# Kernel tuning notes

Measured on AMD Instinct MI355X. Metric: run time of the kernel, lower is better.

Reference implementation:

```python
import jax, jax.numpy as jnp
import numpy as np

HIDDEN = 4096
NUM_HEADS = 32
NUM_KV_HEADS = 8
HEAD_DIM = 128
EPS = 1e-6
ROPE_THETA = 1000000.0
B, S = 4, 1024


def setup_inputs() -> dict:
    key = jax.random.key(0)
    ks = jax.random.split(key, 8)
    sd = 1.0 / np.sqrt(HIDDEN)
    return {
        "hidden_states": jax.random.normal(ks[0], (B, S, HIDDEN), jnp.float32),
        "positions": jnp.broadcast_to(jnp.arange(S, dtype=jnp.int32), (B, S)),
        "wq": jax.random.normal(ks[1], (HIDDEN, NUM_HEADS * HEAD_DIM), jnp.float32) * sd,
        "wk": jax.random.normal(ks[2], (HIDDEN, NUM_KV_HEADS * HEAD_DIM), jnp.float32) * sd,
        "wv": jax.random.normal(ks[3], (HIDDEN, NUM_KV_HEADS * HEAD_DIM), jnp.float32) * sd,
        "wo": jax.random.normal(ks[4], (NUM_HEADS * HEAD_DIM, HIDDEN), jnp.float32) * sd,
        "q_norm_scale": jnp.ones((HEAD_DIM,), jnp.float32),
        "k_norm_scale": jnp.ones((HEAD_DIM,), jnp.float32),
    }


def _rms_norm(x, scale):
    # per-head RMSNorm over last dim (head_dim)
    var = jnp.mean(jnp.square(x), axis=-1, keepdims=True)
    return x * jax.lax.rsqrt(var + EPS) * scale


def _rope_non_neox(x, positions):
    # x: [B, S, H, D]; non-neox (interleaved) RoPE over full head_dim
    inv_freq = 1.0 / (ROPE_THETA ** (jnp.arange(0, HEAD_DIM, 2, dtype=jnp.float32) / HEAD_DIM))
    freqs = positions.astype(jnp.float32)[..., None] * inv_freq  # [B, S, D/2]
    cos = jnp.cos(freqs)[:, :, None, :]  # [B, S, 1, D/2]
    sin = jnp.sin(freqs)[:, :, None, :]
    x1 = x[..., 0::2]
    x2 = x[..., 1::2]
    o1 = x1 * cos - x2 * sin
    o2 = x2 * cos + x1 * sin
    return jnp.stack([o1, o2], axis=-1).reshape(x.shape)


def reference(hidden_states, positions, wq, wk, wv, wo, q_norm_scale, k_norm_scale):
    b, s, _ = hidden_states.shape
    q = (hidden_states @ wq).reshape(b, s, NUM_HEADS, HEAD_DIM)
    k = (hidden_states @ wk).reshape(b, s, NUM_KV_HEADS, HEAD_DIM)
    v = (hidden_states @ wv).reshape(b, s, NUM_KV_HEADS, HEAD_DIM)

    q = _rms_norm(q, q_norm_scale)
    k = _rms_norm(k, k_norm_scale)

    q = _rope_non_neox(q, positions)
    k = _rope_non_neox(k, positions)

    # GQA: expand kv heads to match q heads
    group = NUM_HEADS // NUM_KV_HEADS
    k = jnp.repeat(k, group, axis=2)  # [B, S, NH, D]
    v = jnp.repeat(v, group, axis=2)

    scale = HEAD_DIM ** -0.5
    scores = jnp.einsum("bqhd,bkhd->bhqk", q, k) * scale  # [B, NH, S, S]
    causal = jnp.tril(jnp.ones((s, s), dtype=bool))
    scores = jnp.where(causal, scores, jnp.finfo(scores.dtype).min)
    probs = jax.nn.softmax(scores, axis=-1)
    attn = jnp.einsum("bhqk,bkhd->bqhd", probs, v).reshape(b, s, NUM_HEADS * HEAD_DIM)
    return attn @ wo
```

## Files before the change

kernel.cpp:

```cpp
#include <hip/hip_runtime.h>
#include <hip/hip_bf16.h>
#include <cstdint>

#define HIDDEN 4096
#define NQ 32
#define NKV 8
#define HD 128
#define BB 4
#define SS 1024
#define NTOK (BB*SS)
#define NQKV 6144

typedef __bf16 bf16x8 __attribute__((ext_vector_type(8)));
typedef float f32x4 __attribute__((ext_vector_type(4)));
typedef unsigned short u16;
typedef unsigned int u32;

__device__ __forceinline__ void gload_lds16(const void* g, void* l) {
  __builtin_amdgcn_global_load_lds((const __attribute__((address_space(1))) u32*)g,
                                   (__attribute__((address_space(3))) u32*)l, 16, 0, 0);
}

__device__ __forceinline__ u16 f2bf(float f) {
  u32 x = __float_as_uint(f);
  u32 r = x + 0x7fffu + ((x >> 16) & 1u);
  return (u16)(r >> 16);
}
__device__ __forceinline__ float bf2f(u16 x) {
  u32 v = ((u32)x) << 16;
  return __uint_as_float(v);
}

__global__ void cast_f32_bf16_k(const float4* __restrict__ in, ushort4* __restrict__ out, int n4)
{
  for (int i = blockIdx.x*blockDim.x + threadIdx.x; i < n4; i += gridDim.x*blockDim.x) {
    float4 v = in[i];
    ushort4 o;
    o.x = f2bf(v.x); o.y = f2bf(v.y); o.z = f2bf(v.z); o.w = f2bf(v.w);
    out[i] = o;
  }
}

__global__ __launch_bounds__(256) void transpose_cast(const float* __restrict__ in,
                                                      u16* __restrict__ out, int K, int N)
{
  __shared__ float tile[32][33];
  int n0 = blockIdx.x*32, k0 = blockIdx.y*32;
  int tx = threadIdx.x & 31, ty = threadIdx.x >> 5;
  #pragma unroll
  for (int i=0;i<4;i++) {
    int k = ty + i*8;
    tile[k][tx] = in[(size_t)(k0+k)*N + n0 + tx];
  }
  __syncthreads();
  #pragma unroll
  for (int i=0;i<4;i++) {
    int n = ty + i*8;
    out[(size_t)(n0+n)*K + k0 + tx] = f2bf(tile[tx][n]);
  }
}

__global__ void rope_tab_k(const int* __restrict__ pos, float2* __restrict__ tab)
{
  int i = blockIdx.x*256 + threadIdx.x;
  if (i >= NTOK*64) return;
  int t = i >> 6, j = i & 63;
  float p = (float)pos[t];
  const float l2t = 19.931568569324174f;
  float inv = exp2f(-(float)j * (l2t/64.0f));
  float f = p * inv;
  tab[i] = make_float2(cosf(f), sinf(f));
}

template<int BF16_OUT>
__global__ __launch_bounds__(256, 2) void gemm_bt(const u16* __restrict__ A,
                                                  const u16* __restrict__ Bt,
                                                  void* __restrict__ Cv,
                                                  int M, int N, int K)
{
  __shared__ u16 lA[128*64];
  __shared__ u16 lB[128*64];
  const int m0 = blockIdx.y*128, n0 = blockIdx.x*128;
  const int tid = threadIdx.x;
  const int w = tid >> 6, l = tid & 63;
  const int wr = w >> 1, wc = w & 1;
  const int cl = l & 15, g4 = l >> 4;
  const int lr = l >> 3, gd = l & 7;
  f32x4 acc[4][4] = {};

  for (int k0 = 0; k0 < K; k0 += 64) {
    #pragma unroll
    for (int c2 = 0; c2 < 4; ++c2) {
      int r = w*32 + c2*8 + lr;
      int gs = gd ^ (r & 7);
      gload_lds16(A  + (size_t)(m0+r)*K + k0 + gs*8, &lA[(w*32 + c2*8)*64]);
      gload_lds16(Bt + (size_t)(n0+r)*K + k0 + gs*8, &lB[(w*32 + c2*8)*64]);
    }
    __syncthreads();
    #pragma unroll
    for (int kk = 0; kk < 2; ++kk) {
      bf16x8 af[4], bfr[4];
      #pragma unroll
      for (int i=0;i<4;i++) {
        int ra = wr*64 + i*16 + cl;
        af[i]  = *(const bf16x8*)&lA[ra*64 + ((kk*4+g4) ^ (ra&7))*8];
        int rb = wc*64 + i*16 + cl;
        bfr[i] = *(const bf16x8*)&lB[rb*64 + ((kk*4+g4) ^ (rb&7))*8];
      }
      #pragma unroll
      for (int i=0;i<4;i++)
        #pragma unroll
        for (int j=0;j<4;j++)
          acc[i][j] = __builtin_amdgcn_mfma_f32_16x16x32_bf16(af[i], bfr[j], acc[i][j], 0,0,0);
    }
    __syncthreads();
  }

  #pragma unroll
  for (int i=0;i<4;i++)
    #pragma unroll
    for (int rg=0;rg<4;rg++) {
      size_t row = m0 + wr*64 + i*16 + g4*4 + rg;
      #pragma unroll
      for (int j=0;j<4;j++) {
        size_t col = n0 + wc*64 + j*16 + cl;
        if (BF16_OUT) ((u16*)Cv)[row*N + col] = f2bf(acc[i][j][rg]);
        else          ((float*)Cv)[row*N + col] = acc[i][j][rg];
      }
    }
}

__global__ __launch_bounds__(256) void norm_rope(u16* __restrict__ qkv,
                                                 const float* __restrict__ qsc,
                                                 const float* __restrict__ ksc,
                                                 const float2* __restrict__ tab)
{
  const int t = blockIdx.x;
  const int w = threadIdx.x >> 6, l = threadIdx.x & 63;
  const float2 cs = tab[t*64 + l];
  for (int slot = w; slot < 40; slot += 4) {
    const float* sc = (slot < 32) ? qsc : ksc;
    int col = (slot < 32) ? slot*HD : 4096 + (slot-32)*HD;
    u32* p = (u32*)(qkv + (size_t)t*NQKV + col) + l;
    u32 v = *p;
    float x0 = bf2f((u16)(v & 0xffff)), x1 = bf2f((u16)(v >> 16));
    float ss = x0*x0 + x1*x1;
    ss += __shfl_xor(ss, 1);  ss += __shfl_xor(ss, 2);  ss += __shfl_xor(ss, 4);
    ss += __shfl_xor(ss, 8);  ss += __shfl_xor(ss, 16); ss += __shfl_xor(ss, 32);
    float r = rsqrtf(ss * (1.0f/128.0f) + 1e-6f);
    float y0 = x0 * r * sc[2*l], y1 = x1 * r * sc[2*l+1];
    float o0 = y0*cs.x - y1*cs.y;
    float o1 = y1*cs.x + y0*cs.y;
    *p = (u32)f2bf(o0) | ((u32)f2bf(o1) << 16);
  }
}

__global__ __launch_bounds__(256) void v_transpose(const u16* __restrict__ qkv,
                                                   u16* __restrict__ vt)
{
  __shared__ u16 tile[32][136];
  const int s0 = blockIdx.x*32;
  const int z  = blockIdx.y;
  const int b = z >> 3, kvh = z & 7;
  const int tid = threadIdx.x;
  const int tr = tid >> 4, ln = tid & 15;
  const size_t base = ((size_t)b*SS)*NQKV + 5120 + (size_t)kvh*HD;
  #pragma unroll
  for (int i=0;i<2;i++) {
    int srow = tr + i*16;
    *(bf16x8*)&tile[srow][ln*8] =
        *(const bf16x8*)&qkv[base + (size_t)(s0+srow)*NQKV + ln*8];
  }
  __syncthreads();
  const int dr = tid >> 1, sh = (tid & 1)*16;
  u16 tmp[16];
  #pragma unroll
  for (int j=0;j<16;j++) tmp[j] = tile[sh+j][dr];
  u16* o = vt + ((size_t)z*HD + dr)*SS + s0 + sh;
  *(bf16x8*)o       = *(const bf16x8*)&tmp[0];
  *(bf16x8*)(o + 8) = *(const bf16x8*)&tmp[8];
}

__global__ __launch_bounds__(256, 2) void attn_fwd(const u16* __restrict__ qkv,
                                                   const u16* __restrict__ vt,
                                                   u16* __restrict__ out)
{
  __shared__ u16 Kb[2][64*128];
  __shared__ u16 Vb[2][128*64];
  __shared__ u16 Pl[4][16*64];
  const int qp = blockIdx.x, h = blockIdx.y, b = blockIdx.z;
  const int kvh = h >> 2;
  const int tid = threadIdx.x, w = tid >> 6, l = tid & 63;
  const int cl = l & 15, g4 = l >> 4;
  const float csc = 1.4426950408889634f * 0.08838834764831845f;
  const size_t kbase = ((size_t)b*SS)*NQKV + 4096 + (size_t)kvh*HD;
  const size_t vbase = ((size_t)b*8 + (size_t)kvh)*HD*SS;
  u16* Pw = &Pl[w][0];

  const int kr_l = l >> 4, kg_l = l & 15;
  const int vr_l = l >> 3, vg_l = l & 7;

  #pragma unroll
  for (int t = 0; t < 2; ++t) {
    const int qt = t ? (15 - qp) : qp;
    const int q0 = qt*64;

    bf16x8 qf[4];
    const size_t qrow = ((size_t)b*SS + q0 + w*16 + cl)*NQKV + h*HD;
    #pragma unroll
    for (int kk=0;kk<4;kk++) qf[kk] = *(const bf16x8*)&qkv[qrow + kk*32 + g4*8];

    f32x4 O[8] = {};
    float mrow[4] = {-INFINITY,-INFINITY,-INFINITY,-INFINITY};
    float srow[4] = {0.f,0.f,0.f,0.f};

    const int nch = qt + 1;

    #pragma unroll
    for (int i=0;i<4;i++) {
      int inst = w*4 + i;
      int r = inst*4 + kr_l;
      int g = kg_l ^ (r & 15);
      gload_lds16(qkv + kbase + (size_t)r*NQKV + g*8, &Kb[0][inst*512]);
      int d = inst*8 + vr_l;
      int gv = vg_l ^ (d & 7);
      gload_lds16(vt + vbase + (size_t)d*SS + gv*8, &Vb[0][inst*512]);
    }
    __syncthreads();
    int cur = 0;

    for (int ch = 0; ch < nch; ++ch) {
      const int kv0 = ch*64;
      if (ch + 1 < nch) {
        const size_t knext = kbase + (size_t)(kv0+64)*NQKV;
        const size_t vnext = vbase + (size_t)(kv0+64);
        u16* Kn = &Kb[cur^1][0];
        u16* Vn = &Vb[cur^1][0];
        #pragma unroll
        for (int i=0;i<4;i++) {
          int inst = w*4 + i;
          int r = inst*4 + kr_l;
          int g = kg_l ^ (r & 15);
          gload_lds16(qkv + knext + (size_t)r*NQKV + g*8, Kn + inst*512);
          int d = inst*8 + vr_l;
          int gv = vg_l ^ (d & 7);
          gload_lds16(vt + vnext + (size_t)d*SS + gv*8, Vn + inst*512);
        }
      }
      const u16* Kt  = &Kb[cur][0];
      const u16* Vtl = &Vb[cur][0];
      f32x4 s[4] = {};
      #pragma unroll
      for (int cc=0;cc<4;cc++) {
        const int kro = (cc*16+cl)*128;
        #pragma unroll
        for (int kk=0;kk<4;kk++) {
          bf16x8 kf = *(const bf16x8*)&Kt[kro + (((kk*4+g4) ^ cl))*8];
          s[cc] = __builtin_amdgcn_mfma_f32_16x16x32_bf16(qf[kk], kf, s[cc], 0,0,0);
        }
      }
      float alpha[4];
      #pragma unroll
      for (int rg=0; rg<4; ++rg) {
        const int qr = q0 + w*16 + g4*4 + rg;
        float sv[4];
        #pragma unroll
        for (int cc=0;cc<4;cc++) {
          sv[cc] = s[cc][rg]*csc;
          if (kv0 + cc*16 + cl > qr) sv[cc] = -INFINITY;
        }
        float mx = fmaxf(fmaxf(sv[0],sv[1]), fmaxf(sv[2],sv[3]));
        mx = fmaxf(mx, __shfl_xor(mx,1));
        mx = fmaxf(mx, __shfl_xor(mx,2));
        mx = fmaxf(mx, __shfl_xor(mx,4));
        mx = fmaxf(mx, __shfl_xor(mx,8));
        float mn = fmaxf(mrow[rg], mx);
        float al = exp2f(mrow[rg] - mn);
        mrow[rg] = mn;
        float p0 = exp2f(sv[0]-mn), p1 = exp2f(sv[1]-mn);
        float p2 = exp2f(sv[2]-mn), p3 = exp2f(sv[3]-mn);
        float ps = (p0+p1)+(p2+p3);
        ps += __shfl_xor(ps,1); ps += __shfl_xor(ps,2);
        ps += __shfl_xor(ps,4); ps += __shfl_xor(ps,8);
        srow[rg] = srow[rg]*al + ps;
        alpha[rg] = al;
        const int r = g4*4+rg;
        const int rs = r*64, rx = r&7;
        float pv[4] = {p0,p1,p2,p3};
        #pragma unroll
        for (int cc=0;cc<4;cc++) {
          int c = cc*16+cl;
          Pw[rs + (((c>>3) ^ rx))*8 + (c&7)] = f2bf(pv[cc]);
        }
      }
      #pragma unroll
      for (int dc=0;dc<8;dc++)
        #pragma unroll
        for (int rg=0;rg<4;rg++) O[dc][rg] *= alpha[rg];
      #pragma unroll
      for (int cc2=0;cc2<2;cc2++) {
        bf16x8 pf = *(const bf16x8*)&Pw[cl*64 + (((cc2*4+g4) ^ (cl&7)))*8];
        #pragma unroll
        for (int dc=0;dc<8;dc++) {
          bf16x8 vf = *(const bf16x8*)&Vtl[(dc*16+cl)*64 + (((cc2*4+g4) ^ (cl&7)))*8];
          O[dc] = __builtin_amdgcn_mfma_f32_16x16x32_bf16(pf, vf, O[dc], 0,0,0);
        }
      }
      __syncthreads();
      cur ^= 1;
    }
    #pragma unroll
    for (int rg=0;rg<4;rg++) {
      float inv = 1.0f / srow[rg];
      size_t ob = ((size_t)b*SS + q0 + w*16 + g4*4 + rg)*4096 + (size_t)h*HD;
      #pragma unroll
      for (int dc=0;dc<8;dc++)
        out[ob + dc*16 + cl] = f2bf(O[dc][rg]*inv);
    }
  }
}

extern "C" void kernel_launch(void* const* d_in, const int* in_sizes, int n_in,
                              void* d_out, int out_size, void* d_ws, size_t ws_size,
                              hipStream_t stream)
{
  const float* hid = (const float*)d_in[0];
  const int*   pos = (const int*)d_in[1];
  const float* wq  = (const float*)d_in[2];
  const float* wk  = (const float*)d_in[3];
  const float* wv  = (const float*)d_in[4];
  const float* wo  = (const float*)d_in[5];
  const float* qsc = (const float*)d_in[6];
  const float* ksc = (const float*)d_in[7];

  char* ws = (char*)d_ws;
  size_t off = 0;
  auto alloc = [&](size_t b) -> char* {
    char* p = ws + off;
    off = (off + b + 255) & ~(size_t)255;
    return p;
  };
  u16*    h_bf   = (u16*)   alloc((size_t)NTOK*HIDDEN*2);
  u16*    wqkv_t = (u16*)   alloc((size_t)NQKV*HIDDEN*2);
  u16*    wo_t   = (u16*)   alloc((size_t)HIDDEN*HIDDEN*2);
  u16*    qkv    = (u16*)   alloc((size_t)NTOK*NQKV*2);
  u16*    attn_o = (u16*)   alloc((size_t)NTOK*HIDDEN*2);
  u16*    vtb    = (u16*)   alloc((size_t)BB*NKV*HD*SS*2);
  float2* tab    = (float2*)alloc((size_t)NTOK*64*sizeof(float2));

  cast_f32_bf16_k<<<2048, 256, 0, stream>>>((const float4*)hid, (ushort4*)h_bf, NTOK*HIDDEN/4);
  transpose_cast<<<dim3(HIDDEN/32, HIDDEN/32), 256, 0, stream>>>(wq, wqkv_t, HIDDEN, HIDDEN);
  transpose_cast<<<dim3(1024/32,  HIDDEN/32), 256, 0, stream>>>(wk, wqkv_t + (size_t)4096*HIDDEN, HIDDEN, 1024);
  transpose_cast<<<dim3(1024/32,  HIDDEN/32), 256, 0, stream>>>(wv, wqkv_t + (size_t)5120*HIDDEN, HIDDEN, 1024);
  transpose_cast<<<dim3(HIDDEN/32, HIDDEN/32), 256, 0, stream>>>(wo, wo_t, HIDDEN, HIDDEN);
  rope_tab_k<<<NTOK*64/256, 256, 0, stream>>>(pos, tab);

  gemm_bt<1><<<dim3(NQKV/128, NTOK/128), 256, 0, stream>>>(h_bf, wqkv_t, qkv, NTOK, NQKV, HIDDEN);
  norm_rope<<<NTOK, 256, 0, stream>>>(qkv, qsc, ksc, tab);
  v_transpose<<<dim3(SS/32, BB*NKV), 256, 0, stream>>>(qkv, vtb);
  attn_fwd<<<dim3(8, NQ, BB), 256, 0, stream>>>(qkv, vtb, attn_o);
  gemm_bt<0><<<dim3(HIDDEN/128, NTOK/128), 256, 0, stream>>>(attn_o, wo_t, d_out, NTOK, HIDDEN, HIDDEN);
}
```

Measured before the change: 515.3 us.

## Replace GEMM with 256x256 tile, 8-wave, double-buffered LDS pipeline

Swaps the 128x128 single-buffered GEMM for a 256x256-tile kernel with 512 threads (8 waves, each owning a 128x64 output region). LDS is double-buffered and the next K-tile's global-to-LDS loads are issued between MFMA phases, with s_setprio raising wave priority around the MFMA bursts. The aim is more data reuse per tile and to hide global-load latency behind matrix math. In exchange it uses 128 KB of LDS per block, which limits occupancy, and the grids shrink (384 and 256 blocks), which may leave some CUs idle.

```diff
diff --git a/kernel.cpp b/kernel.cpp
--- a/kernel.cpp
+++ b/kernel.cpp
@@ -73,59 +73,129 @@
 }
 
 template<int BF16_OUT>
-__global__ __launch_bounds__(256, 2) void gemm_bt(const u16* __restrict__ A,
-                                                  const u16* __restrict__ Bt,
-                                                  void* __restrict__ Cv,
-                                                  int M, int N, int K)
-{
-  __shared__ u16 lA[128*64];
-  __shared__ u16 lB[128*64];
-  const int m0 = blockIdx.y*128, n0 = blockIdx.x*128;
+__global__ __launch_bounds__(512, 2) void gemm_bt8(const u16* __restrict__ A,
+                                                   const u16* __restrict__ Bt,
+                                                   void* __restrict__ Cv,
+                                                   int M, int N, int K)
+{
+  __shared__ u16 lA[2][256*64];
+  __shared__ u16 lB[2][256*64];
+  const int m0 = blockIdx.y*256, n0 = blockIdx.x*256;
   const int tid = threadIdx.x;
-  const int w = tid >> 6, l = tid & 63;
-  const int wr = w >> 1, wc = w & 1;
+  const int w = tid >> 6;
+  const int wm = w >> 2, wn = w & 3;
+  const int l = tid & 63;
   const int cl = l & 15, g4 = l >> 4;
-  const int lr = l >> 3, gd = l & 7;
-  f32x4 acc[4][4] = {};
-
-  for (int k0 = 0; k0 < K; k0 += 64) {
-    #pragma unroll
-    for (int c2 = 0; c2 < 4; ++c2) {
-      int r = w*32 + c2*8 + lr;
-      int gs = gd ^ (r & 7);
-      gload_lds16(A  + (size_t)(m0+r)*K + k0 + gs*8, &lA[(w*32 + c2*8)*64]);
-      gload_lds16(Bt + (size_t)(n0+r)*K + k0 + gs*8, &lB[(w*32 + c2*8)*64]);
-    }
+  const int rr = tid >> 3;
+  const int sx = (tid & 7) ^ (rr & 7);
+
+  f32x4 acc[8][4] = {};
+  const int nt = K >> 6;
+
+#define STAGE_A(buf, i, k0v) \
+  gload_lds16(A  + (size_t)(m0 + (i)*64 + rr)*K + (k0v) + sx*8, &lA[buf][((i)*64 + w*8)*64])
+#define STAGE_B(buf, i, k0v) \
+  gload_lds16(Bt + (size_t)(n0 + (i)*64 + rr)*K + (k0v) + sx*8, &lB[buf][((i)*64 + w*8)*64])
+
+  #pragma unroll
+  for (int i=0;i<4;i++) { STAGE_A(0,i,0); STAGE_B(0,i,0); }
+  __syncthreads();
+
+  #pragma unroll 2
+  for (int t = 0; t < nt; ++t) {
+    const int cur = t & 1;
+    const int kn = (t+1) << 6;
+    const u16* At = &lA[cur][0];
+    const u16* Bl = &lB[cur][0];
+    bf16x8 a[4][2], b0[2][2], b1[2][2];
+
+    #pragma unroll
+    for (int fi=0;fi<4;fi++) {
+      const int ra = (wm*128 + fi*16 + cl)*64;
+      #pragma unroll
+      for (int kk=0;kk<2;kk++)
+        a[fi][kk] = *(const bf16x8*)&At[ra + (((kk*4+g4) ^ (cl&7)))*8];
+    }
+    #pragma unroll
+    for (int fj=0;fj<2;fj++) {
+      const int rb = (wn*64 + fj*16 + cl)*64;
+      #pragma unroll
+      for (int kk=0;kk<2;kk++)
+        b0[fj][kk] = *(const bf16x8*)&Bl[rb + (((kk*4+g4) ^ (cl&7)))*8];
+    }
+    if (t+1 < nt) { STAGE_A(cur^1,0,kn); STAGE_A(cur^1,1,kn); STAGE_B(cur^1,0,kn); STAGE_B(cur^1,1,kn); }
     __syncthreads();
-    #pragma unroll
-    for (int kk = 0; kk < 2; ++kk) {
-      bf16x8 af[4], bfr[4];
-      #pragma unroll
-      for (int i=0;i<4;i++) {
-        int ra = wr*64 + i*16 + cl;
-        af[i]  = *(const bf16x8*)&lA[ra*64 + ((kk*4+g4) ^ (ra&7))*8];
-        int rb = wc*64 + i*16 + cl;
-        bfr[i] = *(const bf16x8*)&lB[rb*64 + ((kk*4+g4) ^ (rb&7))*8];
-      }
-      #pragma unroll
-      for (int i=0;i<4;i++)
-        #pragma unroll
-        for (int j=0;j<4;j++)
-          acc[i][j] = __builtin_amdgcn_mfma_f32_16x16x32_bf16(af[i], bfr[j], acc[i][j], 0,0,0);
-    }
+    __builtin_amdgcn_s_setprio(1);
+    #pragma unroll
+    for (int fi=0;fi<4;fi++)
+      #pragma unroll
+      for (int fj=0;fj<2;fj++)
+        #pragma unroll
+        for (int kk=0;kk<2;kk++)
+          acc[fi][fj] = __builtin_amdgcn_mfma_f32_16x16x32_bf16(a[fi][kk], b0[fj][kk], acc[fi][fj], 0,0,0);
+    __builtin_amdgcn_s_setprio(0);
+
+    #pragma unroll
+    for (int fj=0;fj<2;fj++) {
+      const int rb = (wn*64 + (fj+2)*16 + cl)*64;
+      #pragma unroll
+      for (int kk=0;kk<2;kk++)
+        b1[fj][kk] = *(const bf16x8*)&Bl[rb + (((kk*4+g4) ^ (cl&7)))*8];
+    }
+    if (t+1 < nt) { STAGE_A(cur^1,2,kn); STAGE_A(cur^1,3,kn); STAGE_B(cur^1,2,kn); STAGE_B(cur^1,3,kn); }
     __syncthreads();
-  }
-
-  #pragma unroll
-  for (int i=0;i<4;i++)
+    __builtin_amdgcn_s_setprio(1);
+    #pragma unroll
+    for (int fi=0;fi<4;fi++)
+      #pragma unroll
+      for (int fj=0;fj<2;fj++)
+        #pragma unroll
+        for (int kk=0;kk<2;kk++)
+          acc[fi][fj+2] = __builtin_amdgcn_mfma_f32_16x16x32_bf16(a[fi][kk], b1[fj][kk], acc[fi][fj+2], 0,0,0);
+    __builtin_amdgcn_s_setprio(0);
+
+    #pragma unroll
+    for (int fi=0;fi<4;fi++) {
+      const int ra = (wm*128 + 64 + fi*16 + cl)*64;
+      #pragma unroll
+      for (int kk=0;kk<2;kk++)
+        a[fi][kk] = *(const bf16x8*)&At[ra + (((kk*4+g4) ^ (cl&7)))*8];
+    }
+    __syncthreads();
+    __builtin_amdgcn_s_setprio(1);
+    #pragma unroll
+    for (int fi=0;fi<4;fi++)
+      #pragma unroll
+      for (int fj=0;fj<2;fj++)
+        #pragma unroll
+        for (int kk=0;kk<2;kk++)
+          acc[fi+4][fj+2] = __builtin_amdgcn_mfma_f32_16x16x32_bf16(a[fi][kk], b1[fj][kk], acc[fi+4][fj+2], 0,0,0);
+    __builtin_amdgcn_s_setprio(0);
+
+    __builtin_amdgcn_s_setprio(1);
+    #pragma unroll
+    for (int fi=0;fi<4;fi++)
+      #pragma unroll
+      for (int fj=0;fj<2;fj++)
+        #pragma unroll
+        for (int kk=0;kk<2;kk++)
+          acc[fi+4][fj] = __builtin_amdgcn_mfma_f32_16x16x32_bf16(a[fi][kk], b0[fj][kk], acc[fi+4][fj], 0,0,0);
+    __builtin_amdgcn_s_setprio(0);
+    __syncthreads();
+  }
+#undef STAGE_A
+#undef STAGE_B
+
+  #pragma unroll
+  for (int am=0;am<8;am++)
     #pragma unroll
     for (int rg=0;rg<4;rg++) {
-      size_t row = m0 + wr*64 + i*16 + g4*4 + rg;
-      #pragma unroll
-      for (int j=0;j<4;j++) {
-        size_t col = n0 + wc*64 + j*16 + cl;
-        if (BF16_OUT) ((u16*)Cv)[row*N + col] = f2bf(acc[i][j][rg]);
-        else          ((float*)Cv)[row*N + col] = acc[i][j][rg];
+      const size_t row = m0 + wm*128 + (am>>2)*64 + (am&3)*16 + g4*4 + rg;
+      #pragma unroll
+      for (int an=0;an<4;an++) {
+        const size_t col = n0 + wn*64 + an*16 + cl;
+        if (BF16_OUT) ((u16*)Cv)[row*N + col] = f2bf(acc[am][an][rg]);
+        else          ((float*)Cv)[row*N + col] = acc[am][an][rg];
       }
     }
 }
@@ -355,9 +425,9 @@
   transpose_cast<<<dim3(HIDDEN/32, HIDDEN/32), 256, 0, stream>>>(wo, wo_t, HIDDEN, HIDDEN);
   rope_tab_k<<<NTOK*64/256, 256, 0, stream>>>(pos, tab);
 
-  gemm_bt<1><<<dim3(NQKV/128, NTOK/128), 256, 0, stream>>>(h_bf, wqkv_t, qkv, NTOK, NQKV, HIDDEN);
+  gemm_bt8<1><<<dim3(NQKV/256, NTOK/256), 512, 0, stream>>>(h_bf, wqkv_t, qkv, NTOK, NQKV, HIDDEN);
   norm_rope<<<NTOK, 256, 0, stream>>>(qkv, qsc, ksc, tab);
   v_transpose<<<dim3(SS/32, BB*NKV), 256, 0, stream>>>(qkv, vtb);
   attn_fwd<<<dim3(8, NQ, BB), 256, 0, stream>>>(qkv, vtb, attn_o);
-  gemm_bt<0><<<dim3(HIDDEN/128, NTOK/128), 256, 0, stream>>>(attn_o, wo_t, d_out, NTOK, HIDDEN, HIDDEN);
-}
+  gemm_bt8<0><<<dim3(HIDDEN/256, NTOK/256), 512, 0, stream>>>(attn_o, wo_t, d_out, NTOK, HIDDEN, HIDDEN);
+}
```

After: 696.2 us. +35.1%, slower.

## Replace GEMM with 256x256 8-wave double-buffered ping-pong pipelined kernel

Applied to the files above, without the earlier changes.

Swaps the 128x128 single-buffered 4-wave GEMM for a 256x256 tile kernel with 8 waves and double-buffered LDS. Loads for the next K-tile are issued in quarters between MFMA phases, and s_setprio plus explicit vmcnt waits overlap global-to-LDS traffic with matrix math. The larger tile raises reuse per loaded byte. In exchange LDS use grows to 128KB per block, which caps occupancy, and fewer blocks are launched (384 and 256), which may underfill the CUs.

```diff
diff --git a/kernel.cpp b/kernel.cpp
--- a/kernel.cpp
+++ b/kernel.cpp
@@ -73,59 +73,110 @@
 }
 
 template<int BF16_OUT>
-__global__ __launch_bounds__(256, 2) void gemm_bt(const u16* __restrict__ A,
-                                                  const u16* __restrict__ Bt,
-                                                  void* __restrict__ Cv,
-                                                  int M, int N, int K)
-{
-  __shared__ u16 lA[128*64];
-  __shared__ u16 lB[128*64];
-  const int m0 = blockIdx.y*128, n0 = blockIdx.x*128;
+__global__ __launch_bounds__(512, 2) void gemm8p(const u16* __restrict__ A,
+                                                 const u16* __restrict__ Bt,
+                                                 void* __restrict__ Cv,
+                                                 int M, int N, int K)
+{
+  __shared__ u16 lA[2][2][128*64];
+  __shared__ u16 lB[2][2][128*64];
+  const int m0 = blockIdx.y*256, n0 = blockIdx.x*256;
   const int tid = threadIdx.x;
   const int w = tid >> 6, l = tid & 63;
-  const int wr = w >> 1, wc = w & 1;
+  const int wm = w >> 2, wn = w & 3;
   const int cl = l & 15, g4 = l >> 4;
-  const int lr = l >> 3, gd = l & 7;
-  f32x4 acc[4][4] = {};
-
-  for (int k0 = 0; k0 < K; k0 += 64) {
-    #pragma unroll
-    for (int c2 = 0; c2 < 4; ++c2) {
-      int r = w*32 + c2*8 + lr;
-      int gs = gd ^ (r & 7);
-      gload_lds16(A  + (size_t)(m0+r)*K + k0 + gs*8, &lA[(w*32 + c2*8)*64]);
-      gload_lds16(Bt + (size_t)(n0+r)*K + k0 + gs*8, &lB[(w*32 + c2*8)*64]);
-    }
-    __syncthreads();
-    #pragma unroll
-    for (int kk = 0; kk < 2; ++kk) {
-      bf16x8 af[4], bfr[4];
-      #pragma unroll
-      for (int i=0;i<4;i++) {
-        int ra = wr*64 + i*16 + cl;
-        af[i]  = *(const bf16x8*)&lA[ra*64 + ((kk*4+g4) ^ (ra&7))*8];
-        int rb = wc*64 + i*16 + cl;
-        bfr[i] = *(const bf16x8*)&lB[rb*64 + ((kk*4+g4) ^ (rb&7))*8];
-      }
-      #pragma unroll
-      for (int i=0;i<4;i++)
-        #pragma unroll
-        for (int j=0;j<4;j++)
-          acc[i][j] = __builtin_amdgcn_mfma_f32_16x16x32_bf16(af[i], bfr[j], acc[i][j], 0,0,0);
-    }
-    __syncthreads();
-  }
-
-  #pragma unroll
-  for (int i=0;i<4;i++)
+  const int sr = l >> 3;
+  const int sg = (l & 7) ^ sr;
+  const u16* Ab = A  + (size_t)m0*K;
+  const u16* Bb = Bt + (size_t)n0*K;
+
+  f32x4 acc[8][4] = {};
+  const int nt = K >> 6;
+
+#define STG_A(buf, half, kt) do { \
+    gload_lds16(Ab + (size_t)((half)*128 +      w*8 + sr)*K + (kt)*64 + sg*8, &lA[buf][half][(     w*8)*64]); \
+    gload_lds16(Ab + (size_t)((half)*128 + 64 + w*8 + sr)*K + (kt)*64 + sg*8, &lA[buf][half][(64 + w*8)*64]); \
+  } while(0)
+#define STG_B(buf, half, kt) do { \
+    gload_lds16(Bb + (size_t)((half)*128 +      w*8 + sr)*K + (kt)*64 + sg*8, &lB[buf][half][(     w*8)*64]); \
+    gload_lds16(Bb + (size_t)((half)*128 + 64 + w*8 + sr)*K + (kt)*64 + sg*8, &lB[buf][half][(64 + w*8)*64]); \
+  } while(0)
+
+#define RD_A(dst, buf, half) \
+    _Pragma("unroll") for (int fi=0;fi<4;fi++) { \
+      const int ra = (wm*64 + fi*16 + cl)*64; \
+      _Pragma("unroll") for (int kk=0;kk<2;kk++) \
+        dst[fi][kk] = *(const bf16x8*)&lA[buf][half][ra + (((kk*4+g4) ^ (cl&7)))*8]; \
+    }
+#define RD_B(dst, buf, half) \
+    _Pragma("unroll") for (int fj=0;fj<2;fj++) { \
+      const int rb = (wn*32 + fj*16 + cl)*64; \
+      _Pragma("unroll") for (int kk=0;kk<2;kk++) \
+        dst[fj][kk] = *(const bf16x8*)&lB[buf][half][rb + (((kk*4+g4) ^ (cl&7)))*8]; \
+    }
+#define MFMA_Q(ai, aj, afrag, bfrag) \
+    __builtin_amdgcn_s_setprio(1); \
+    _Pragma("unroll") for (int fi=0;fi<4;fi++) \
+      _Pragma("unroll") for (int fj=0;fj<2;fj++) \
+        _Pragma("unroll") for (int kk=0;kk<2;kk++) \
+          acc[(ai)+fi][(aj)+fj] = __builtin_amdgcn_mfma_f32_16x16x32_bf16(afrag[fi][kk], bfrag[fj][kk], acc[(ai)+fi][(aj)+fj], 0,0,0); \
+    __builtin_amdgcn_s_setprio(0);
+#define BAR() { __builtin_amdgcn_s_barrier(); __builtin_amdgcn_sched_barrier(0); }
+
+  STG_A(0,0,0); STG_B(0,0,0); STG_A(0,1,0); STG_B(0,1,0);
+  asm volatile("s_waitcnt vmcnt(4)" ::: "memory");
+  BAR();
+
+  for (int t = 0; t < nt; ++t) {
+    const int cur = t & 1, nxt = cur ^ 1;
+    const int kn = t + 1;
+    const bool pf = (kn < nt);
+    bf16x8 aF[4][2], bL[2][2], bH[2][2];
+
+    RD_A(aF, cur, 0);
+    RD_B(bL, cur, 0);
+    if (pf) STG_A(nxt, 0, kn);
+    BAR();
+    MFMA_Q(0, 0, aF, bL);
+    if (pf) { asm volatile("s_waitcnt vmcnt(2)" ::: "memory"); }
+    else    { asm volatile("s_waitcnt vmcnt(0)" ::: "memory"); }
+    BAR();
+
+    RD_B(bH, cur, 1);
+    if (pf) STG_B(nxt, 0, kn);
+    BAR();
+    MFMA_Q(0, 2, aF, bH);
+    BAR();
+
+    RD_A(aF, cur, 1);
+    if (pf) STG_A(nxt, 1, kn);
+    BAR();
+    MFMA_Q(4, 2, aF, bH);
+    BAR();
+
+    if (pf) STG_B(nxt, 1, kn);
+    BAR();
+    MFMA_Q(4, 0, aF, bL);
+    if (pf) { asm volatile("s_waitcnt vmcnt(4)" ::: "memory"); }
+    BAR();
+  }
+#undef STG_A
+#undef STG_B
+#undef RD_A
+#undef RD_B
+#undef MFMA_Q
+#undef BAR
+
+  #pragma unroll
+  for (int am=0;am<8;am++)
     #pragma unroll
     for (int rg=0;rg<4;rg++) {
-      size_t row = m0 + wr*64 + i*16 + g4*4 + rg;
-      #pragma unroll
-      for (int j=0;j<4;j++) {
-        size_t col = n0 + wc*64 + j*16 + cl;
-        if (BF16_OUT) ((u16*)Cv)[row*N + col] = f2bf(acc[i][j][rg]);
-        else          ((float*)Cv)[row*N + col] = acc[i][j][rg];
+      const size_t row = m0 + (am>>2)*128 + wm*64 + (am&3)*16 + g4*4 + rg;
+      #pragma unroll
+      for (int an=0;an<4;an++) {
+        const size_t col = n0 + (an>>1)*128 + wn*32 + (an&1)*16 + cl;
+        if (BF16_OUT) ((u16*)Cv)[row*N + col] = f2bf(acc[am][an][rg]);
+        else          ((float*)Cv)[row*N + col] = acc[am][an][rg];
       }
     }
 }
@@ -355,9 +406,9 @@
   transpose_cast<<<dim3(HIDDEN/32, HIDDEN/32), 256, 0, stream>>>(wo, wo_t, HIDDEN, HIDDEN);
   rope_tab_k<<<NTOK*64/256, 256, 0, stream>>>(pos, tab);
 
-  gemm_bt<1><<<dim3(NQKV/128, NTOK/128), 256, 0, stream>>>(h_bf, wqkv_t, qkv, NTOK, NQKV, HIDDEN);
+  gemm8p<1><<<dim3(NQKV/256, NTOK/256), 512, 0, stream>>>(h_bf, wqkv_t, qkv, NTOK, NQKV, HIDDEN);
   norm_rope<<<NTOK, 256, 0, stream>>>(qkv, qsc, ksc, tab);
   v_transpose<<<dim3(SS/32, BB*NKV), 256, 0, stream>>>(qkv, vtb);
   attn_fwd<<<dim3(8, NQ, BB), 256, 0, stream>>>(qkv, vtb, attn_o);
-  gemm_bt<0><<<dim3(HIDDEN/128, NTOK/128), 256, 0, stream>>>(attn_o, wo_t, d_out, NTOK, HIDDEN, HIDDEN);
-}
+  gemm8p<0><<<dim3(HIDDEN/256, NTOK/256), 512, 0, stream>>>(attn_o, wo_t, d_out, NTOK, HIDDEN, HIDDEN);
+}
```

Result: slower. 543.2 us (+5.4%).

## Replace GEMM with 256x256-tile double-buffered kernel and XCD-aware block swizzle

Applied to the files above, without the earlier changes.

Swaps the 128x128 single-buffered bf16 GEMM for a 256x256-tile kernel with 512 threads. It prefetches K-tiles two steps ahead into double-buffered LDS, using raw s_waitcnt and barriers to overlap loads with MFMA work. Block indices are remapped so consecutive tiles land on the same XCD chiplet, which should improve L2 reuse. The larger tile raises arithmetic intensity, but it uses 128KB of LDS and 128 accumulator registers per thread. That may limit occupancy, and the grids are small (384 and 256 blocks), which risks poor load balance across 256 CUs.

```diff
diff --git a/kernel.cpp b/kernel.cpp
--- a/kernel.cpp
+++ b/kernel.cpp
@@ -73,59 +73,107 @@
 }
 
 template<int BF16_OUT>
-__global__ __launch_bounds__(256, 2) void gemm_bt(const u16* __restrict__ A,
-                                                  const u16* __restrict__ Bt,
-                                                  void* __restrict__ Cv,
-                                                  int M, int N, int K)
-{
-  __shared__ u16 lA[128*64];
-  __shared__ u16 lB[128*64];
-  const int m0 = blockIdx.y*128, n0 = blockIdx.x*128;
+__global__ __launch_bounds__(512, 2) void gemm2b(const u16* __restrict__ A,
+                                                 const u16* __restrict__ Bt,
+                                                 void* __restrict__ Cv,
+                                                 int M, int N, int K, int gx)
+{
+  __shared__ u16 lA[2][256*64];
+  __shared__ u16 lB[2][256*64];
+  const int nwg = gridDim.x;
+  const int cpx = nwg >> 3;
+  const int swz = (blockIdx.x & 7)*cpx + (blockIdx.x >> 3);
+  const int m0 = (swz / gx)*256, n0 = (swz % gx)*256;
+
   const int tid = threadIdx.x;
   const int w = tid >> 6, l = tid & 63;
-  const int wr = w >> 1, wc = w & 1;
+  const int wm = w >> 2, wn = w & 3;
   const int cl = l & 15, g4 = l >> 4;
-  const int lr = l >> 3, gd = l & 7;
-  f32x4 acc[4][4] = {};
-
-  for (int k0 = 0; k0 < K; k0 += 64) {
-    #pragma unroll
-    for (int c2 = 0; c2 < 4; ++c2) {
-      int r = w*32 + c2*8 + lr;
-      int gs = gd ^ (r & 7);
-      gload_lds16(A  + (size_t)(m0+r)*K + k0 + gs*8, &lA[(w*32 + c2*8)*64]);
-      gload_lds16(Bt + (size_t)(n0+r)*K + k0 + gs*8, &lB[(w*32 + c2*8)*64]);
-    }
-    __syncthreads();
-    #pragma unroll
-    for (int kk = 0; kk < 2; ++kk) {
-      bf16x8 af[4], bfr[4];
-      #pragma unroll
-      for (int i=0;i<4;i++) {
-        int ra = wr*64 + i*16 + cl;
-        af[i]  = *(const bf16x8*)&lA[ra*64 + ((kk*4+g4) ^ (ra&7))*8];
-        int rb = wc*64 + i*16 + cl;
-        bfr[i] = *(const bf16x8*)&lB[rb*64 + ((kk*4+g4) ^ (rb&7))*8];
-      }
-      #pragma unroll
-      for (int i=0;i<4;i++)
-        #pragma unroll
-        for (int j=0;j<4;j++)
-          acc[i][j] = __builtin_amdgcn_mfma_f32_16x16x32_bf16(af[i], bfr[j], acc[i][j], 0,0,0);
-    }
-    __syncthreads();
-  }
-
-  #pragma unroll
-  for (int i=0;i<4;i++)
+  const int sr = l >> 3;
+  const int sg = (l & 7) ^ sr;
+  const u16* Ab = A  + (size_t)m0*K;
+  const u16* Bb = Bt + (size_t)n0*K;
+
+  f32x4 acc[8][4] = {};
+  const int nt = K >> 6;
+
+#define STG_TILE(buf, kt) do { \
+    const size_t ko = (size_t)(kt)*64; \
+    _Pragma("unroll") for (int j=0;j<4;j++) { \
+      const int na = w*4 + j; \
+      gload_lds16(Ab + (size_t)(na*8 + sr)*K + ko + sg*8, &lA[buf][na*512]); \
+      gload_lds16(Bb + (size_t)(na*8 + sr)*K + ko + sg*8, &lB[buf][na*512]); \
+    } \
+  } while(0)
+#define BARRIER() asm volatile("s_barrier" ::: "memory")
+
+  STG_TILE(0, 0);
+  STG_TILE(1, 1);
+  asm volatile("s_waitcnt vmcnt(8)" ::: "memory");
+  BARRIER();
+
+  for (int t = 0; t < nt; ++t) {
+    const int cur = t & 1;
+    bf16x8 aF[4][2], bF[4][2];
+
+    #pragma unroll
+    for (int fi=0;fi<4;fi++) {
+      const int ra = wm*128 + fi*16 + cl;
+      #pragma unroll
+      for (int kk=0;kk<2;kk++)
+        aF[fi][kk] = *(const bf16x8*)&lA[cur][ra*64 + (((kk*4+g4) ^ (cl&7)))*8];
+    }
+    #pragma unroll
+    for (int fj=0;fj<4;fj++) {
+      const int rb = wn*64 + fj*16 + cl;
+      #pragma unroll
+      for (int kk=0;kk<2;kk++)
+        bF[fj][kk] = *(const bf16x8*)&lB[cur][rb*64 + (((kk*4+g4) ^ (cl&7)))*8];
+    }
+    #pragma unroll
+    for (int fi=0;fi<4;fi++)
+      #pragma unroll
+      for (int fj=0;fj<4;fj++)
+        #pragma unroll
+        for (int kk=0;kk<2;kk++)
+          acc[fi][fj] = __builtin_amdgcn_mfma_f32_16x16x32_bf16(aF[fi][kk], bF[fj][kk], acc[fi][fj], 0,0,0);
+    #pragma unroll
+    for (int fi=0;fi<4;fi++) {
+      const int ra = wm*128 + 64 + fi*16 + cl;
+      #pragma unroll
+      for (int kk=0;kk<2;kk++)
+        aF[fi][kk] = *(const bf16x8*)&lA[cur][ra*64 + (((kk*4+g4) ^ (cl&7)))*8];
+    }
+    #pragma unroll
+    for (int fi=0;fi<4;fi++)
+      #pragma unroll
+      for (int fj=0;fj<4;fj++)
+        #pragma unroll
+        for (int kk=0;kk<2;kk++)
+          acc[fi+4][fj] = __builtin_amdgcn_mfma_f32_16x16x32_bf16(aF[fi][kk], bF[fj][kk], acc[fi+4][fj], 0,0,0);
+
+    BARRIER();
+    if (t+2 < nt) {
+      STG_TILE(cur, t+2);
+      asm volatile("s_waitcnt vmcnt(8)" ::: "memory");
+    } else if (t+1 < nt) {
+      asm volatile("s_waitcnt vmcnt(0)" ::: "memory");
+    }
+    BARRIER();
+  }
+#undef STG_TILE
+#undef BARRIER
+
+  #pragma unroll
+  for (int fi=0;fi<8;fi++)
     #pragma unroll
     for (int rg=0;rg<4;rg++) {
-      size_t row = m0 + wr*64 + i*16 + g4*4 + rg;
-      #pragma unroll
-      for (int j=0;j<4;j++) {
-        size_t col = n0 + wc*64 + j*16 + cl;
-        if (BF16_OUT) ((u16*)Cv)[row*N + col] = f2bf(acc[i][j][rg]);
-        else          ((float*)Cv)[row*N + col] = acc[i][j][rg];
+      const size_t row = m0 + wm*128 + fi*16 + g4*4 + rg;
+      #pragma unroll
+      for (int fj=0;fj<4;fj++) {
+        const size_t col = n0 + wn*64 + fj*16 + cl;
+        if (BF16_OUT) ((u16*)Cv)[row*N + col] = f2bf(acc[fi][fj][rg]);
+        else          ((float*)Cv)[row*N + col] = acc[fi][fj][rg];
       }
     }
 }
@@ -355,9 +403,9 @@
   transpose_cast<<<dim3(HIDDEN/32, HIDDEN/32), 256, 0, stream>>>(wo, wo_t, HIDDEN, HIDDEN);
   rope_tab_k<<<NTOK*64/256, 256, 0, stream>>>(pos, tab);
 
-  gemm_bt<1><<<dim3(NQKV/128, NTOK/128), 256, 0, stream>>>(h_bf, wqkv_t, qkv, NTOK, NQKV, HIDDEN);
+  gemm2b<1><<<(NQKV/256)*(NTOK/256), 512, 0, stream>>>(h_bf, wqkv_t, qkv, NTOK, NQKV, HIDDEN, NQKV/256);
   norm_rope<<<NTOK, 256, 0, stream>>>(qkv, qsc, ksc, tab);
   v_transpose<<<dim3(SS/32, BB*NKV), 256, 0, stream>>>(qkv, vtb);
   attn_fwd<<<dim3(8, NQ, BB), 256, 0, stream>>>(qkv, vtb, attn_o);
-  gemm_bt<0><<<dim3(HIDDEN/128, NTOK/128), 256, 0, stream>>>(attn_o, wo_t, d_out, NTOK, HIDDEN, HIDDEN);
-}
+  gemm2b<0><<<(HIDDEN/256)*(NTOK/256), 512, 0, stream>>>(attn_o, wo_t, d_out, NTOK, HIDDEN, HIDDEN, HIDDEN/256);
+}
```

Measured after the change: 562.6 us. 1.09x slower.
